# Performance work log

Measured on AMD Instinct MI355X. Metric: run time of the kernel, lower is better.

## Reference

```python
import jax, jax.numpy as jnp
import numpy as np

B, S, N = 1, 128, 256
C_IN, C_H, C_OUT = 256, 32, 128
EPS = 1e-5


def setup_inputs() -> dict:
    key = jax.random.key(0)
    k_m, k_wa, k_wb, k_wo = jax.random.split(key, 4)
    m = jax.random.normal(k_m, (B, S, N, C_IN), dtype=jnp.float32)
    mask = jnp.ones((B, S, N), dtype=jnp.float32)
    gamma = jnp.ones((C_IN,), dtype=jnp.float32)
    beta = jnp.zeros((C_IN,), dtype=jnp.float32)
    # nn.Linear weights are (out, in)
    Wa = jax.random.normal(k_wa, (C_H, C_IN), dtype=jnp.float32) / np.sqrt(C_IN).astype(np.float32)
    Wb = jax.random.normal(k_wb, (C_H, C_IN), dtype=jnp.float32) / np.sqrt(C_IN).astype(np.float32)
    # proj_o is final_init (zeros) in the source; use small random weights so the
    # baseline output is non-trivial for correctness checking.
    Wo = jax.random.normal(k_wo, (C_OUT, C_H * C_H), dtype=jnp.float32) / np.sqrt(C_H * C_H).astype(np.float32)
    bo = jnp.zeros((C_OUT,), dtype=jnp.float32)
    return {"m": m, "mask": mask, "gamma": gamma, "beta": beta,
            "Wa": Wa, "Wb": Wb, "Wo": Wo, "bo": bo}


def reference(m, mask, gamma, beta, Wa, Wb, Wo, bo):
    # LayerNorm over c_in
    mu = jnp.mean(m, axis=-1, keepdims=True)
    var = jnp.mean((m - mu) ** 2, axis=-1, keepdims=True)
    mn = (m - mu) * jax.lax.rsqrt(var + EPS) * gamma + beta  # (B,S,N,c_in)

    mk = mask[..., None]  # (B,S,N,1)
    a = jnp.einsum('bsni,hi->bsnh', mn, Wa) * mk  # (B,S,N,c_h)
    b = jnp.einsum('bsni,hi->bsnh', mn, Wb) * mk  # (B,S,N,c_h)

    # pairwise mask count over S, clamped to >= 1
    num_mask = jnp.clip(jnp.einsum('bsi,bsj->bij', mask, mask), 1.0, None)  # (B,N,N)

    # outer-product mean over the sequence dim
    z = jnp.einsum('bsic,bsjd->bijcd', a, b)  # (B,N,N,c_h,c_h)
    z = z.reshape(z.shape[0], z.shape[1], z.shape[2], C_H * C_H)
    z = z / num_mask[..., None]

    return jnp.einsum('bijk,ok->bijo', z, Wo) + bo  # (B,N,N,c_out)
```

## Files before the change

kernel.cpp:

```cpp
#include <hip/hip_runtime.h>

#define S_DIM 128
#define N_DIM 256
#define CIN   256
#define CH    32
#define COUT  128

typedef __attribute__((ext_vector_type(8))) short bf16x8;
typedef __attribute__((ext_vector_type(4))) float f32x4;

__device__ __forceinline__ unsigned short f2bf(float f) {
  union { float f; unsigned int u; } v; v.f = f;
  unsigned int u = v.u;
  return (unsigned short)((u + 0x7FFFu + ((u >> 16) & 1u)) >> 16);
}

__global__ __launch_bounds__(256) void k0_ln_prep(
    const float* __restrict__ m, const float* __restrict__ mask,
    const float* __restrict__ gamma, const float* __restrict__ beta,
    const float* __restrict__ Wa, const float* __restrict__ Wb,
    const float* __restrict__ Wo,
    float* __restrict__ rnm, unsigned short* __restrict__ wab_bf,
    unsigned short* __restrict__ wo2, unsigned short* __restrict__ mn_g) {
  const int b = blockIdx.x, t = threadIdx.x;
  if (b < 2048) {
    const int w = t >> 6, l = t & 63;
    const int rbase = b * 16 + w * 4;
    const float4 g4 = *(const float4*)(gamma + l * 4);
    const float4 b4 = *(const float4*)(beta + l * 4);
    float4 v[4];
    #pragma unroll
    for (int rr = 0; rr < 4; rr++)
      v[rr] = *(const float4*)(m + (size_t)(rbase + rr) * CIN + l * 4);
    #pragma unroll
    for (int rr = 0; rr < 4; rr++) {
      float sum = v[rr].x + v[rr].y + v[rr].z + v[rr].w;
      float sq  = v[rr].x * v[rr].x + v[rr].y * v[rr].y +
                  v[rr].z * v[rr].z + v[rr].w * v[rr].w;
      #pragma unroll
      for (int off = 32; off > 0; off >>= 1) {
        sum += __shfl_down(sum, off);
        sq  += __shfl_down(sq, off);
      }
      sum = __shfl(sum, 0); sq = __shfl(sq, 0);
      const float mu = sum * (1.0f / CIN);
      const float var = fmaxf(sq * (1.0f / CIN) - mu * mu, 0.0f);
      const float rs = rsqrtf(var + 1e-5f);
      const float mk = mask[rbase + rr];
      ushort4 p;
      p.x = f2bf(((v[rr].x - mu) * rs * g4.x + b4.x) * mk);
      p.y = f2bf(((v[rr].y - mu) * rs * g4.y + b4.y) * mk);
      p.z = f2bf(((v[rr].z - mu) * rs * g4.z + b4.z) * mk);
      p.w = f2bf(((v[rr].w - mu) * rs * g4.w + b4.w) * mk);
      *(ushort4*)(mn_g + (size_t)(rbase + rr) * CIN + l * 4) = p;
    }
  } else if (b < 2112) {
    const int r = b - 2048;
    const float* src = (r < 32) ? (Wa + r * CIN) : (Wb + (r - 32) * CIN);
    wab_bf[r * CIN + t] = f2bf(src[t]);
  } else if (b < 2240) {
    const int r = b - 2112;
    #pragma unroll
    for (int q = 0; q < 4; q++) {
      const int f = r * 1024 + q * 256 + t;
      const int e = f & 7, l = (f >> 3) & 63, kk = (f >> 9) & 31, ot = f >> 14;
      const int kp = kk * 32 + (l >> 4) * 8 + e;
      const int c = kp & 31, d = kp >> 5;
      const int o = ot * 16 + (l & 15);
      wo2[f] = f2bf(Wo[o * 1024 + c * 32 + d]);
    }
  } else {
    const int i = b - 2240;
    float acc = 0.f;
    #pragma unroll 8
    for (int s = 0; s < S_DIM; s++)
      acc += mask[s * N_DIM + i] * mask[s * N_DIM + t];
    acc = fmaxf(acc, 1.0f);
    rnm[i * N_DIM + t] = 1.0f / acc;
  }
}

__global__ __launch_bounds__(256) void proj_kernel(
    const unsigned short* __restrict__ mn_g,
    const unsigned short* __restrict__ wab_bf,
    unsigned short* __restrict__ a_t, unsigned short* __restrict__ b_t) {
  __shared__ __align__(16) unsigned short mn[32][264];
  const int i = blockIdx.x;
  const int s0 = blockIdx.y * 32;
  const int t = threadIdx.x, w = t >> 6, l = t & 63;
  const int lq = l >> 4, lr = l & 15;

  #pragma unroll
  for (int rr = 0; rr < 8; rr++) {
    const int r = w * 8 + rr;
    const size_t rid = (size_t)(s0 + r) * N_DIM + i;
    *(ushort4*)(&mn[r][l * 4]) = *(const ushort4*)(mn_g + rid * CIN + l * 4);
  }
  __syncthreads();

  const int wm = w & 1;
  const int n2 = w >> 1;
  f32x4 acc0 = {0.f, 0.f, 0.f, 0.f}, acc1 = {0.f, 0.f, 0.f, 0.f};
  #pragma unroll
  for (int ks = 0; ks < 8; ks++) {
    const int k0 = ks * 32 + lq * 8;
    const bf16x8 af = *(const bf16x8*)(&mn[wm * 16 + lr][k0]);
    const unsigned short* wrow = wab_bf + (n2 * 32 + lr) * CIN + k0;
    const bf16x8 bf0 = *(const bf16x8*)(wrow);
    const bf16x8 bf1 = *(const bf16x8*)(wrow + 16 * CIN);
    acc0 = __builtin_amdgcn_mfma_f32_16x16x32_bf16(af, bf0, acc0, 0, 0, 0);
    acc1 = __builtin_amdgcn_mfma_f32_16x16x32_bf16(af, bf1, acc1, 0, 0, 0);
  }

  unsigned short* dst = (n2 == 0) ? a_t : b_t;
  const int scol = s0 + wm * 16 + lq * 4;
  ushort4 q0, q1;
  q0.x = f2bf(acc0[0]); q0.y = f2bf(acc0[1]); q0.z = f2bf(acc0[2]); q0.w = f2bf(acc0[3]);
  q1.x = f2bf(acc1[0]); q1.y = f2bf(acc1[1]); q1.z = f2bf(acc1[2]); q1.w = f2bf(acc1[3]);
  *(ushort4*)(dst + ((size_t)(i * CH + lr)) * S_DIM + scol) = q0;
  *(ushort4*)(dst + ((size_t)(i * CH + 16 + lr)) * S_DIM + scol) = q1;
}

__global__ __launch_bounds__(1024, 4) void fused_kernel(
    const unsigned short* __restrict__ a_t, const unsigned short* __restrict__ b_t,
    const unsigned short* __restrict__ wo2, const float* __restrict__ rnm,
    const float* __restrict__ bo, float* __restrict__ out) {
  extern __shared__ __align__(16) unsigned short smem[];
  unsigned short* sA = smem;
  unsigned short* sB = smem + 32768;
  unsigned short* sZ = smem;

  const int t = threadIdx.x, w = t >> 6, l = t & 63;
  const int lq = l >> 4, lr = l & 15;
  const int lin = blockIdx.x;
  const int li = lin >> 3;
  const int by = ((lin & 7) << 2) | (li >> 5);
  const int bx = li & 31;

  const unsigned short* srcA = a_t + (size_t)bx * 32768;
  const unsigned short* srcB = b_t + (size_t)by * 32768;
  #pragma unroll
  for (int it = 0; it < 4; it++) {
    const int idx = it * 1024 + t;
    const int r = idx >> 4, g = idx & 15;
    const int dst = r * 128 + ((g ^ (r & 15)) * 8);
    *(bf16x8*)(&sA[dst]) = *(const bf16x8*)(srcA + idx * 8);
    *(bf16x8*)(&sB[dst]) = *(const bf16x8*)(srcB + idx * 8);
  }
  __syncthreads();

  const int wy = (w >> 2) * 64, wx = (w & 3) * 64;
  f32x4 acc[4][4];
  #pragma unroll
  for (int a = 0; a < 4; a++)
    #pragma unroll
    for (int c = 0; c < 4; c++) acc[a][c] = (f32x4){0.f, 0.f, 0.f, 0.f};

  #pragma unroll
  for (int ks = 0; ks < 4; ks++) {
    const int g0 = ks * 4 + lq;
    bf16x8 afr[4], bfr[4];
    #pragma unroll
    for (int a = 0; a < 4; a++) {
      const int ra = wy + a * 16 + lr;
      afr[a] = *(const bf16x8*)(&sA[ra * 128 + ((g0 ^ (ra & 15)) * 8)]);
      const int rb = wx + a * 16 + lr;
      bfr[a] = *(const bf16x8*)(&sB[rb * 128 + ((g0 ^ (rb & 15)) * 8)]);
    }
    #pragma unroll
    for (int a = 0; a < 4; a++)
      #pragma unroll
      for (int c = 0; c < 4; c++)
        acc[a][c] = __builtin_amdgcn_mfma_f32_16x16x32_bf16(afr[a], bfr[c], acc[a][c], 0, 0, 0);
  }
  __syncthreads();

  #pragma unroll
  for (int a = 0; a < 4; a++) {
    #pragma unroll
    for (int c = 0; c < 4; c++) {
      const int zrb = wy + a * 16 + lq * 4;
      const int zc  = wx + c * 16 + lr;
      const int pair = (zrb >> 5) * 8 + (zc >> 5);
      const int off = (zc & 31) * 32 + (zrb & 31);
      const int g = off >> 3;
      const int gp = (g & ~7) | ((g ^ (g >> 3) ^ pair) & 7);
      ushort4 q;
      q.x = f2bf(acc[a][c][0]); q.y = f2bf(acc[a][c][1]);
      q.z = f2bf(acc[a][c][2]); q.w = f2bf(acc[a][c][3]);
      *(ushort4*)(&sZ[pair * 1024 + gp * 8 + (off & 7)]) = q;
    }
  }
  __syncthreads();

  const int ot = w >> 1, wm2 = w & 1;
  const int p0 = wm2 * 32 + lr, p1 = p0 + 16;
  const unsigned short* wbase = wo2 + (size_t)ot * 16384 + (size_t)l * 8;
  f32x4 oa[2][2];
  oa[0][0] = oa[0][1] = oa[1][0] = oa[1][1] = (f32x4){0.f, 0.f, 0.f, 0.f};
  #pragma unroll 4
  for (int kk = 0; kk < 32; kk++) {
    const int g = kk * 4 + lq;
    const int gp0 = (g & ~7) | ((g ^ (g >> 3) ^ p0) & 7);
    const int gp1 = (g & ~7) | ((g ^ (g >> 3) ^ p1) & 7);
    const bf16x8 wf = *(const bf16x8*)(wbase + kk * 512);
    const bf16x8 z0 = *(const bf16x8*)(&sZ[p0 * 1024 + gp0 * 8]);
    const bf16x8 z1 = *(const bf16x8*)(&sZ[p1 * 1024 + gp1 * 8]);
    oa[0][kk & 1] = __builtin_amdgcn_mfma_f32_16x16x32_bf16(z0, wf, oa[0][kk & 1], 0, 0, 0);
    oa[1][kk & 1] = __builtin_amdgcn_mfma_f32_16x16x32_bf16(z1, wf, oa[1][kk & 1], 0, 0, 0);
  }

  const int o = ot * 16 + lr;
  const float bov = bo[o];
  #pragma unroll
  for (int f = 0; f < 2; f++) {
    #pragma unroll
    for (int r = 0; r < 4; r++) {
      const int pair = wm2 * 32 + f * 16 + lq * 4 + r;
      const int ii = bx * 8 + (pair >> 3);
      const int jj = by * 8 + (pair & 7);
      const float sc = rnm[ii * N_DIM + jj];
      out[((size_t)(ii * N_DIM + jj)) * COUT + o] =
          (oa[f][0][r] + oa[f][1][r]) * sc + bov;
    }
  }
}

extern "C" void kernel_launch(void* const* d_in, const int* in_sizes, int n_in,
                              void* d_out, int out_size, void* d_ws, size_t ws_size,
                              hipStream_t stream) {
  const float* m     = (const float*)d_in[0];
  const float* mask  = (const float*)d_in[1];
  const float* gamma = (const float*)d_in[2];
  const float* beta  = (const float*)d_in[3];
  const float* Wa    = (const float*)d_in[4];
  const float* Wb    = (const float*)d_in[5];
  const float* Wo    = (const float*)d_in[6];
  const float* bo    = (const float*)d_in[7];
  float* out = (float*)d_out;

  char* ws = (char*)d_ws;
  float*          rnm    = (float*)(ws);
  unsigned short* wo2    = (unsigned short*)(ws + 262144);
  unsigned short* wab_bf = (unsigned short*)(ws + 524288);
  unsigned short* a_t    = (unsigned short*)(ws + 557056);
  unsigned short* b_t    = (unsigned short*)(ws + 2654208);
  unsigned short* mn_g   = (unsigned short*)(ws + 4751360);

  hipFuncSetAttribute((const void*)fused_kernel,
                      hipFuncAttributeMaxDynamicSharedMemorySize, 131072);

  k0_ln_prep<<<2496, 256, 0, stream>>>(m, mask, gamma, beta, Wa, Wb, Wo,
                                       rnm, wab_bf, wo2, mn_g);
  proj_kernel<<<dim3(256, 4), 256, 0, stream>>>(mn_g, wab_bf, a_t, b_t);
  fused_kernel<<<1024, 1024, 131072, stream>>>(a_t, b_t, wo2, rnm, bo, out);
}
```

Before: 155.7 us.

## Load outer-product operands directly from global, drop LDS staging and swizzled grid

The outer-product GEMM now reads its A and B fragments straight from global memory instead of first copying them into swizzled LDS, which removes a staging pass and two barriers. The second GEMM is remapped so each wave reads one Z fragment and two Wo fragments, where before it read two Z fragments and one Wo fragment. This cuts LDS reads but doubles the global weight loads per wave. The grid changes from a 1D swizzled order to a plain 2D (32,32) order, which drops the L2-locality block mapping. The risks are more global and L2 traffic, uncoalesced 16-byte strided loads, and worse cache reuse.

```diff
diff --git a/kernel.cpp b/kernel.cpp
--- a/kernel.cpp
+++ b/kernel.cpp
@@ -125,31 +125,15 @@
     const unsigned short* __restrict__ a_t, const unsigned short* __restrict__ b_t,
     const unsigned short* __restrict__ wo2, const float* __restrict__ rnm,
     const float* __restrict__ bo, float* __restrict__ out) {
-  extern __shared__ __align__(16) unsigned short smem[];
-  unsigned short* sA = smem;
-  unsigned short* sB = smem + 32768;
-  unsigned short* sZ = smem;
+  extern __shared__ __align__(16) unsigned short sZ[];
 
   const int t = threadIdx.x, w = t >> 6, l = t & 63;
   const int lq = l >> 4, lr = l & 15;
-  const int lin = blockIdx.x;
-  const int li = lin >> 3;
-  const int by = ((lin & 7) << 2) | (li >> 5);
-  const int bx = li & 31;
-
+  const int bx = blockIdx.x, by = blockIdx.y;
+
+  const int wy = (w >> 2) * 64, wx = (w & 3) * 64;
   const unsigned short* srcA = a_t + (size_t)bx * 32768;
   const unsigned short* srcB = b_t + (size_t)by * 32768;
-  #pragma unroll
-  for (int it = 0; it < 4; it++) {
-    const int idx = it * 1024 + t;
-    const int r = idx >> 4, g = idx & 15;
-    const int dst = r * 128 + ((g ^ (r & 15)) * 8);
-    *(bf16x8*)(&sA[dst]) = *(const bf16x8*)(srcA + idx * 8);
-    *(bf16x8*)(&sB[dst]) = *(const bf16x8*)(srcB + idx * 8);
-  }
-  __syncthreads();
-
-  const int wy = (w >> 2) * 64, wx = (w & 3) * 64;
   f32x4 acc[4][4];
   #pragma unroll
   for (int a = 0; a < 4; a++)
@@ -158,14 +142,12 @@
 
   #pragma unroll
   for (int ks = 0; ks < 4; ks++) {
-    const int g0 = ks * 4 + lq;
+    const int kcol = ks * 32 + lq * 8;
     bf16x8 afr[4], bfr[4];
     #pragma unroll
     for (int a = 0; a < 4; a++) {
-      const int ra = wy + a * 16 + lr;
-      afr[a] = *(const bf16x8*)(&sA[ra * 128 + ((g0 ^ (ra & 15)) * 8)]);
-      const int rb = wx + a * 16 + lr;
-      bfr[a] = *(const bf16x8*)(&sB[rb * 128 + ((g0 ^ (rb & 15)) * 8)]);
+      afr[a] = *(const bf16x8*)(srcA + (wy + a * 16 + lr) * 128 + kcol);
+      bfr[a] = *(const bf16x8*)(srcB + (wx + a * 16 + lr) * 128 + kcol);
     }
     #pragma unroll
     for (int a = 0; a < 4; a++)
@@ -173,7 +155,6 @@
       for (int c = 0; c < 4; c++)
         acc[a][c] = __builtin_amdgcn_mfma_f32_16x16x32_bf16(afr[a], bfr[c], acc[a][c], 0, 0, 0);
   }
-  __syncthreads();
 
   #pragma unroll
   for (int a = 0; a < 4; a++) {
@@ -193,30 +174,30 @@
   }
   __syncthreads();
 
-  const int ot = w >> 1, wm2 = w & 1;
-  const int p0 = wm2 * 32 + lr, p1 = p0 + 16;
-  const unsigned short* wbase = wo2 + (size_t)ot * 16384 + (size_t)l * 8;
+  const int pg = w & 3, og = w >> 2;
+  const int p = pg * 16 + lr;
+  const unsigned short* wbase0 = wo2 + (size_t)(og * 2) * 16384 + (size_t)l * 8;
+  const unsigned short* wbase1 = wbase0 + 16384;
   f32x4 oa[2][2];
   oa[0][0] = oa[0][1] = oa[1][0] = oa[1][1] = (f32x4){0.f, 0.f, 0.f, 0.f};
   #pragma unroll 4
   for (int kk = 0; kk < 32; kk++) {
     const int g = kk * 4 + lq;
-    const int gp0 = (g & ~7) | ((g ^ (g >> 3) ^ p0) & 7);
-    const int gp1 = (g & ~7) | ((g ^ (g >> 3) ^ p1) & 7);
-    const bf16x8 wf = *(const bf16x8*)(wbase + kk * 512);
-    const bf16x8 z0 = *(const bf16x8*)(&sZ[p0 * 1024 + gp0 * 8]);
-    const bf16x8 z1 = *(const bf16x8*)(&sZ[p1 * 1024 + gp1 * 8]);
-    oa[0][kk & 1] = __builtin_amdgcn_mfma_f32_16x16x32_bf16(z0, wf, oa[0][kk & 1], 0, 0, 0);
-    oa[1][kk & 1] = __builtin_amdgcn_mfma_f32_16x16x32_bf16(z1, wf, oa[1][kk & 1], 0, 0, 0);
-  }
-
-  const int o = ot * 16 + lr;
-  const float bov = bo[o];
+    const int gp = (g & ~7) | ((g ^ (g >> 3) ^ p) & 7);
+    const bf16x8 zf = *(const bf16x8*)(&sZ[p * 1024 + gp * 8]);
+    const bf16x8 w0 = *(const bf16x8*)(wbase0 + kk * 512);
+    const bf16x8 w1 = *(const bf16x8*)(wbase1 + kk * 512);
+    oa[0][kk & 1] = __builtin_amdgcn_mfma_f32_16x16x32_bf16(zf, w0, oa[0][kk & 1], 0, 0, 0);
+    oa[1][kk & 1] = __builtin_amdgcn_mfma_f32_16x16x32_bf16(zf, w1, oa[1][kk & 1], 0, 0, 0);
+  }
+
   #pragma unroll
   for (int f = 0; f < 2; f++) {
+    const int o = (og * 2 + f) * 16 + lr;
+    const float bov = bo[o];
     #pragma unroll
     for (int r = 0; r < 4; r++) {
-      const int pair = wm2 * 32 + f * 16 + lq * 4 + r;
+      const int pair = pg * 16 + lq * 4 + r;
       const int ii = bx * 8 + (pair >> 3);
       const int jj = by * 8 + (pair & 7);
       const float sc = rnm[ii * N_DIM + jj];
@@ -253,5 +234,5 @@
   k0_ln_prep<<<2496, 256, 0, stream>>>(m, mask, gamma, beta, Wa, Wb, Wo,
                                        rnm, wab_bf, wo2, mn_g);
   proj_kernel<<<dim3(256, 4), 256, 0, stream>>>(mn_g, wab_bf, a_t, b_t);
-  fused_kernel<<<1024, 1024, 131072, stream>>>(a_t, b_t, wo2, rnm, bo, out);
-}
+  fused_kernel<<<dim3(32, 32), 1024, 131072, stream>>>(a_t, b_t, wo2, rnm, bo, out);
+}
```

After: 209.1 us. 34.3% more time.
